# Optimization experiments

Hardware: AMD Instinct MI355X
Metric: run time of the kernel (lower is better)

Reference implementation:

```python
import jax, jax.numpy as jnp
import numpy as np

B, H_HIST, S_DIM, HID, G, K, A = 1024, 16384, 32, 64, 10, 4, 8


def setup_inputs() -> dict:
    key = jax.random.key(0)
    ks = jax.random.split(key, 12)
    inp = {
        'state_batch': jax.random.normal(ks[0], (B, S_DIM), jnp.float32),
        'state_history_batch': jax.random.normal(ks[1], (H_HIST, S_DIM), jnp.float32),
        'joint_action_history_batch': jax.random.normal(ks[2], (H_HIST, G, A), jnp.float32),
        # per-abstract-agent encoder MLP: Linear(S->H) + ReLU, Linear(H->H) + ReLU, Linear(H->H) + ReLU
        'W0': jax.random.normal(ks[3], (K, S_DIM, HID), jnp.float32) / np.sqrt(S_DIM),
        'b0': jax.random.normal(ks[4], (K, HID), jnp.float32) * 0.01,
        'W1': jax.random.normal(ks[5], (K, HID, HID), jnp.float32) / np.sqrt(HID),
        'b1': jax.random.normal(ks[6], (K, HID), jnp.float32) * 0.01,
        'W2': jax.random.normal(ks[7], (K, HID, HID), jnp.float32) / np.sqrt(HID),
        'b2': jax.random.normal(ks[8], (K, HID), jnp.float32) * 0.01,
        'assignment_matrix': jnp.ones((G, K), jnp.float32),
    }
    return inp


def _encode(x, W0, b0, W1, b1, W2, b2):
    # x: [N, S_DIM] shared across K encoders -> [K, N, HID]
    h = jax.nn.relu(jnp.einsum('ni,kio->kno', x, W0) + b0[:, None, :])
    h = jax.nn.relu(jnp.einsum('kni,kio->kno', h, W1) + b1[:, None, :])
    h = jax.nn.relu(jnp.einsum('kni,kio->kno', h, W2) + b2[:, None, :])
    return h


def reference(state_batch, state_history_batch, joint_action_history_batch,
              W0, b0, W1, b1, W2, b2, assignment_matrix):
    enc_s = _encode(state_batch, W0, b0, W1, b1, W2, b2)            # [K, B, HID]
    enc_h = _encode(state_history_batch, W0, b0, W1, b1, W2, b2)    # [K, H, HID]
    # per (abstract agent k, batch item b): softmax over history of <enc_h, enc_s>
    attn = jax.nn.softmax(jnp.einsum('khd,kbd->kbh', enc_h, enc_s), axis=-1)  # [K, B, H]
    # weighted action aggregation: [H,G,A] contracted over H
    abs_pred = jnp.einsum('kbh,hga->kbga', attn, joint_action_history_batch)  # [K, B, G, A]
    soft_assign = jax.nn.softmax(assignment_matrix, axis=-1)                  # [G, K]
    out = jnp.einsum('gk,kbga->bga', soft_assign, abs_pred)                   # [B, G, A]
    return out
```

## Files before the change

kernel.cpp:

```cpp
#include <hip/hip_runtime.h>
#include <stdint.h>

#define B_SZ 1024
#define H_SZ 16384
#define SD   32
#define HID  64
#define G_SZ 10
#define K_SZ 4
#define A_SZ 8
#define VA   80

typedef float f32x4  __attribute__((ext_vector_type(4)));
typedef short bf16x8 __attribute__((ext_vector_type(8)));

__device__ inline short f2bf(float a) {
    unsigned u = __float_as_uint(a);
    return (short)((u + 0x7FFFu + ((u >> 16) & 1u)) >> 16);
}
__device__ inline float bf2f(short s) {
    return __uint_as_float(((unsigned)(unsigned short)s) << 16);
}
__device__ inline void split_bf(float v, short& hi, short& lo) {
    hi = f2bf(v);
    lo = f2bf(v - bf2f(hi));
}
__device__ inline int cvt_pk_bf16(float a, float b) {
    int r;
    asm("v_cvt_pk_bf16_f32 %0, %1, %2" : "=v"(r) : "v"(a), "v"(b));
    return r;
}

__global__ __launch_bounds__(256) void k_prep(
    const float* __restrict__ W0, const float* __restrict__ W1,
    const float* __restrict__ W2,
    short* __restrict__ w0h, short* __restrict__ w0l,
    short* __restrict__ w1h, short* __restrict__ w1l,
    short* __restrict__ w2h, short* __restrict__ w2l)
{
    int idx = blockIdx.x * 256 + threadIdx.x;
    short hh, ll;
    if (idx < 8192) {
        int k = idx >> 11, j = (idx >> 5) & 63, i = idx & 31;
        split_bf(W0[k * 2048 + i * 64 + j], hh, ll);
        w0h[idx] = hh; w0l[idx] = ll;
    } else if (idx < 24576) {
        int d = idx - 8192;
        int k = d >> 12, j = (d >> 6) & 63, i = d & 63;
        split_bf(W1[k * 4096 + i * 64 + j], hh, ll);
        w1h[d] = hh; w1l[d] = ll;
    } else if (idx < 40960) {
        int d = idx - 24576;
        int k = d >> 12, j = (d >> 6) & 63, i = d & 63;
        split_bf(W2[k * 4096 + i * 64 + j], hh, ll);
        w2h[d] = hh; w2l[d] = ll;
    }
}

__global__ __launch_bounds__(256, 2) void k_encode(
    const float* __restrict__ state, const float* __restrict__ hist,
    const float* __restrict__ act,
    const short* __restrict__ w0th, const short* __restrict__ w0tl,
    const short* __restrict__ w1th, const short* __restrict__ w1tl,
    const short* __restrict__ w2th, const short* __restrict__ w2tl,
    const float* __restrict__ b0, const float* __restrict__ b1,
    const float* __restrict__ b2,
    short* __restrict__ enc_s_h, short* __restrict__ enc_s_l,
    short* __restrict__ kf_h, short* __restrict__ kf_l,
    short* __restrict__ vf_h, short* __restrict__ vf_l)
{
    __shared__ __align__(16) short smem[28672];
    const int bid = blockIdx.x;
    const int t = threadIdx.x;

    if (bid >= 1088) {
        short* tile_h = smem;
        short* tile_l = smem + 10752;
        const int h0 = (bid - 1088) * 128;
        for (int i = 0; i < 40; ++i) {
            int idx = t + i * 256;
            float v = act[(size_t)h0 * VA + idx];
            int h = idx / VA, c = idx - h * VA;
            short hh, ll; split_bf(v, hh, ll);
            tile_h[h * 84 + c] = hh;
            tile_l[h * 84 + c] = ll;
        }
        __syncthreads();
        for (int i = 0; i < 5; ++i) {
            int j = t + i * 256;
            int va = j >> 4, hc = j & 15;
            union { short s[8]; uint4 v; } uh, ul;
            #pragma unroll
            for (int uu = 0; uu < 8; ++uu) {
                uh.s[uu] = tile_h[(hc * 8 + uu) * 84 + va];
                ul.s[uu] = tile_l[(hc * 8 + uu) * 84 + va];
            }
            int vtile = (h0 >> 5) + (hc >> 2);
            int lanep = ((hc & 3) << 4) | (va & 15);
            size_t a = (size_t)vtile * 2560 + (va >> 4) * 512 + lanep * 8;
            *(uint4*)(vf_h + a) = uh.v;
            *(uint4*)(vf_l + a) = ul.v;
        }
        return;
    }

    const int k = bid / 272;
    const int tl = bid % 272;
    const bool is_state = (tl < 16);
    const float qscale = is_state ? 1.44269504f : 1.0f;
    const float* X;
    short *dst_h = nullptr, *dst_l = nullptr;
    if (is_state) {
        X = state + (size_t)tl * 64 * SD;
        dst_h = enc_s_h + ((size_t)k * B_SZ + tl * 64) * HID;
        dst_l = enc_s_l + ((size_t)k * B_SZ + tl * 64) * HID;
    } else {
        X = hist + (size_t)(tl - 16) * 64 * SD;
    }

    short* xt_h  = smem;
    short* xt_l  = smem + 2560;
    short* wt0_h = smem + 5120;
    short* wt0_l = smem + 7680;
    short* hb2_h = smem;
    short* hb2_l = smem + 4608;
    short* wt1_h = smem + 10240;
    short* wt1_l = smem + 14848;
    short* ot_h  = smem + 10240;
    short* ot_l  = smem + 14848;
    short* hb1_h = smem + 19456;
    short* hb1_l = smem + 24064;
    short* wt2_h = smem + 19456;
    short* wt2_l = smem + 24064;

    {
        int r = t >> 2, c0 = (t & 3) * 8;
        const float* src = X + r * SD + c0;
        #pragma unroll
        for (int u = 0; u < 8; ++u) {
            short hh, ll; split_bf(src[u], hh, ll);
            xt_h[r * 40 + c0 + u] = hh;
            xt_l[r * 40 + c0 + u] = ll;
        }
    }
    {
        int jj = t >> 2, i0 = (t & 3) * 8;
        *(uint4*)(wt0_h + jj * 40 + i0) = *(const uint4*)(w0th + k * 2048 + jj * 32 + i0);
        *(uint4*)(wt0_l + jj * 40 + i0) = *(const uint4*)(w0tl + k * 2048 + jj * 32 + i0);
    }
    {
        int jj = t >> 2, i0 = (t & 3) * 16;
        *(uint4*)(wt1_h + jj * 72 + i0)     = *(const uint4*)(w1th + k * 4096 + jj * 64 + i0);
        *(uint4*)(wt1_h + jj * 72 + i0 + 8) = *(const uint4*)(w1th + k * 4096 + jj * 64 + i0 + 8);
        *(uint4*)(wt1_l + jj * 72 + i0)     = *(const uint4*)(w1tl + k * 4096 + jj * 64 + i0);
        *(uint4*)(wt1_l + jj * 72 + i0 + 8) = *(const uint4*)(w1tl + k * 4096 + jj * 64 + i0 + 8);
    }
    __syncthreads();

    const int w = t >> 6, l15 = t & 15, quad = (t >> 4) & 3;
    const f32x4 fz = {0.f, 0.f, 0.f, 0.f};

    {
        bf16x8 xa_h = *(const bf16x8*)(xt_h + (w * 16 + l15) * 40 + quad * 8);
        bf16x8 xa_l = *(const bf16x8*)(xt_l + (w * 16 + l15) * 40 + quad * 8);
        const float* b0k = b0 + k * HID;
        #pragma unroll
        for (int tt = 0; tt < 4; ++tt) {
            bf16x8 wf_h = *(const bf16x8*)(wt0_h + (l15 + 16 * tt) * 40 + quad * 8);
            bf16x8 wf_l = *(const bf16x8*)(wt0_l + (l15 + 16 * tt) * 40 + quad * 8);
            f32x4 c = __builtin_amdgcn_mfma_f32_16x16x32_bf16(xa_h, wf_h, fz, 0, 0, 0);
            c = __builtin_amdgcn_mfma_f32_16x16x32_bf16(xa_l, wf_h, c, 0, 0, 0);
            c = __builtin_amdgcn_mfma_f32_16x16x32_bf16(xa_h, wf_l, c, 0, 0, 0);
            float bias = b0k[l15 + 16 * tt];
            #pragma unroll
            for (int r = 0; r < 4; ++r) {
                float f = fmaxf(c[r] + bias, 0.f);
                short hh, ll; split_bf(f, hh, ll);
                hb1_h[(w * 16 + quad * 4 + r) * 72 + l15 + 16 * tt] = hh;
                hb1_l[(w * 16 + quad * 4 + r) * 72 + l15 + 16 * tt] = ll;
            }
        }
    }
    __syncthreads();
    {
        bf16x8 ha0_h = *(const bf16x8*)(hb1_h + (w * 16 + l15) * 72 + quad * 8);
        bf16x8 ha0_l = *(const bf16x8*)(hb1_l + (w * 16 + l15) * 72 + quad * 8);
        bf16x8 ha1_h = *(const bf16x8*)(hb1_h + (w * 16 + l15) * 72 + 32 + quad * 8);
        bf16x8 ha1_l = *(const bf16x8*)(hb1_l + (w * 16 + l15) * 72 + 32 + quad * 8);
        const float* b1k = b1 + k * HID;
        #pragma unroll
        for (int tt = 0; tt < 4; ++tt) {
            bf16x8 wfa_h = *(const bf16x8*)(wt1_h + (l15 + 16 * tt) * 72 + quad * 8);
            bf16x8 wfa_l = *(const bf16x8*)(wt1_l + (l15 + 16 * tt) * 72 + quad * 8);
            bf16x8 wfb_h = *(const bf16x8*)(wt1_h + (l15 + 16 * tt) * 72 + 32 + quad * 8);
            bf16x8 wfb_l = *(const bf16x8*)(wt1_l + (l15 + 16 * tt) * 72 + 32 + quad * 8);
            f32x4 c = __builtin_amdgcn_mfma_f32_16x16x32_bf16(ha0_h, wfa_h, fz, 0, 0, 0);
            c = __builtin_amdgcn_mfma_f32_16x16x32_bf16(ha1_h, wfb_h, c, 0, 0, 0);
            c = __builtin_amdgcn_mfma_f32_16x16x32_bf16(ha0_l, wfa_h, c, 0, 0, 0);
            c = __builtin_amdgcn_mfma_f32_16x16x32_bf16(ha1_l, wfb_h, c, 0, 0, 0);
            c = __builtin_amdgcn_mfma_f32_16x16x32_bf16(ha0_h, wfa_l, c, 0, 0, 0);
            c = __builtin_amdgcn_mfma_f32_16x16x32_bf16(ha1_h, wfb_l, c, 0, 0, 0);
            float bias = b1k[l15 + 16 * tt];
            #pragma unroll
            for (int r = 0; r < 4; ++r) {
                float f = fmaxf(c[r] + bias, 0.f);
                short hh, ll; split_bf(f, hh, ll);
                hb2_h[(w * 16 + quad * 4 + r) * 72 + l15 + 16 * tt] = hh;
                hb2_l[(w * 16 + quad * 4 + r) * 72 + l15 + 16 * tt] = ll;
            }
        }
    }
    __syncthreads();
    {
        int jj = t >> 2, i0 = (t & 3) * 16;
        *(uint4*)(wt2_h + jj * 72 + i0)     = *(const uint4*)(w2th + k * 4096 + jj * 64 + i0);
        *(uint4*)(wt2_h + jj * 72 + i0 + 8) = *(const uint4*)(w2th + k * 4096 + jj * 64 + i0 + 8);
        *(uint4*)(wt2_l + jj * 72 + i0)     = *(const uint4*)(w2tl + k * 4096 + jj * 64 + i0);
        *(uint4*)(wt2_l + jj * 72 + i0 + 8) = *(const uint4*)(w2tl + k * 4096 + jj * 64 + i0 + 8);
    }
    __syncthreads();
    {
        bf16x8 ha0_h = *(const bf16x8*)(hb2_h + (w * 16 + l15) * 72 + quad * 8);
        bf16x8 ha0_l = *(const bf16x8*)(hb2_l + (w * 16 + l15) * 72 + quad * 8);
        bf16x8 ha1_h = *(const bf16x8*)(hb2_h + (w * 16 + l15) * 72 + 32 + quad * 8);
        bf16x8 ha1_l = *(const bf16x8*)(hb2_l + (w * 16 + l15) * 72 + 32 + quad * 8);
        const float* b2k = b2 + k * HID;
        #pragma unroll
        for (int tt = 0; tt < 4; ++tt) {
            bf16x8 wfa_h = *(const bf16x8*)(wt2_h + (l15 + 16 * tt) * 72 + quad * 8);
            bf16x8 wfa_l = *(const bf16x8*)(wt2_l + (l15 + 16 * tt) * 72 + quad * 8);
            bf16x8 wfb_h = *(const bf16x8*)(wt2_h + (l15 + 16 * tt) * 72 + 32 + quad * 8);
            bf16x8 wfb_l = *(const bf16x8*)(wt2_l + (l15 + 16 * tt) * 72 + 32 + quad * 8);
            f32x4 c = __builtin_amdgcn_mfma_f32_16x16x32_bf16(ha0_h, wfa_h, fz, 0, 0, 0);
            c = __builtin_amdgcn_mfma_f32_16x16x32_bf16(ha1_h, wfb_h, c, 0, 0, 0);
            c = __builtin_amdgcn_mfma_f32_16x16x32_bf16(ha0_l, wfa_h, c, 0, 0, 0);
            c = __builtin_amdgcn_mfma_f32_16x16x32_bf16(ha1_l, wfb_h, c, 0, 0, 0);
            c = __builtin_amdgcn_mfma_f32_16x16x32_bf16(ha0_h, wfa_l, c, 0, 0, 0);
            c = __builtin_amdgcn_mfma_f32_16x16x32_bf16(ha1_h, wfb_l, c, 0, 0, 0);
            float bias = b2k[l15 + 16 * tt];
            #pragma unroll
            for (int r = 0; r < 4; ++r) {
                float f = fmaxf(c[r] + bias, 0.f) * qscale;
                short hh, ll; split_bf(f, hh, ll);
                int row = w * 16 + quad * 4 + r;
                int col = l15 + 16 * tt;
                ot_h[row * 72 + col] = hh;
                ot_l[row * 72 + col] = ll;
            }
        }
    }
    __syncthreads();
    if (is_state) {
        #pragma unroll
        for (int u = 0; u < 2; ++u) {
            int id = t * 2 + u;
            int row = id >> 3, c0 = (id & 7) * 8;
            *(uint4*)(dst_h + row * HID + c0) = *(const uint4*)(ot_h + row * 72 + c0);
            *(uint4*)(dst_l + row * HID + c0) = *(const uint4*)(ot_l + row * 72 + c0);
        }
    } else {
        const int ktbase = k * 512 + (tl - 16) * 2;
        #pragma unroll
        for (int u = 0; u < 2; ++u) {
            int id = t * 2 + u;
            int kt2 = id >> 8;
            int f2 = (id >> 6) & 3;
            int lanep = id & 63;
            int hl = kt2 * 32 + ((f2 >> 1) & 1) * 16 + (lanep & 15);
            int c0 = (f2 & 1) * 32 + ((lanep >> 4) & 3) * 8;
            size_t a = (size_t)(ktbase + kt2) * 2048 + f2 * 512 + (size_t)lanep * 8;
            *(uint4*)(kf_h + a) = *(const uint4*)(ot_h + hl * 72 + c0);
            *(uint4*)(kf_l + a) = *(const uint4*)(ot_l + hl * 72 + c0);
        }
    }
}

template<int NCt>
__global__ __launch_bounds__(256, 2) void k_flash(
    const short* __restrict__ enc_s_h, const short* __restrict__ enc_s_l,
    const short* __restrict__ kf_h, const short* __restrict__ kf_l,
    const short* __restrict__ vf_h, const short* __restrict__ vf_l,
    float* __restrict__ Pm, float* __restrict__ Pl, float* __restrict__ Pacc)
{
    constexpr int CHt = H_SZ / NCt;
    constexpr int NT = CHt / 32;
    static_assert(NT % 2 == 0, "NT must be even for 2x unroll");

    const int bid = blockIdx.x;
    const int r8 = bid & 7, j = bid >> 3;
    const int mtile = j & 7, grp = j >> 3;
    const int idx = grp * 8 + r8;
    const int k = idx / NCt, chunk = idx % NCt;
    const int t = threadIdx.x, w = t >> 6, lane = t & 63;
    const int l15 = t & 15, quad = (t >> 4) & 3;
    const int q0 = mtile * 128 + w * 32;
    const f32x4 fz = {0.f, 0.f, 0.f, 0.f};

    bf16x8 qh[2][2], ql[2][2];
    #pragma unroll
    for (int sub = 0; sub < 2; ++sub)
        #pragma unroll
        for (int kb = 0; kb < 2; ++kb) {
            size_t off = ((size_t)k * B_SZ + q0 + sub * 16 + l15) * HID + kb * 32 + quad * 8;
            qh[sub][kb] = *(const bf16x8*)(enc_s_h + off);
            ql[sub][kb] = *(const bf16x8*)(enc_s_l + off);
        }

    f32x4 acc[2][5];
    #pragma unroll
    for (int s = 0; s < 2; ++s)
        #pragma unroll
        for (int tt = 0; tt < 5; ++tt) acc[s][tt] = fz;
    float mrun[2] = {-__builtin_inff(), -__builtin_inff()};
    float lrun[2] = {0.f, 0.f};

    const int tile0 = chunk * NT;
    const short* kbh = kf_h + ((size_t)(k * 512 + tile0)) * 2048 + lane * 8;
    const short* kbl = kf_l + ((size_t)(k * 512 + tile0)) * 2048 + lane * 8;
    const short* vbh = vf_h + (size_t)tile0 * 2560 + lane * 8;
    const short* vbl = vf_l + (size_t)tile0 * 2560 + lane * 8;

    bf16x8 kA[8], kB[8];
    #pragma unroll
    for (int f = 0; f < 4; ++f) {
        kA[f]     = *(const bf16x8*)(kbh + f * 512);
        kA[4 + f] = *(const bf16x8*)(kbl + f * 512);
    }

    auto body = [&](bf16x8 (&kc)[8], bf16x8 (&kn)[8], int it) {
        bf16x8 vh[5], vl[5];
        const short* vph = vbh + (size_t)it * 2560;
        const short* vpl = vbl + (size_t)it * 2560;
        #pragma unroll
        for (int tt = 0; tt < 3; ++tt) {
            vh[tt] = *(const bf16x8*)(vph + tt * 512);
            vl[tt] = *(const bf16x8*)(vpl + tt * 512);
        }
        if (it + 1 < NT) {
            const short* nph = kbh + (size_t)(it + 1) * 2048;
            const short* npl = kbl + (size_t)(it + 1) * 2048;
            #pragma unroll
            for (int f = 0; f < 4; ++f) {
                kn[f]     = *(const bf16x8*)(nph + f * 512);
                kn[4 + f] = *(const bf16x8*)(npl + f * 512);
            }
        }

        f32x4 S[2][2];
        __builtin_amdgcn_s_setprio(1);
        #pragma unroll
        for (int sub = 0; sub < 2; ++sub) {
            f32x4 c = __builtin_amdgcn_mfma_f32_16x16x32_bf16(kc[0], qh[sub][0], fz, 0, 0, 0);
            c = __builtin_amdgcn_mfma_f32_16x16x32_bf16(kc[1], qh[sub][1], c, 0, 0, 0);
            c = __builtin_amdgcn_mfma_f32_16x16x32_bf16(kc[4], qh[sub][0], c, 0, 0, 0);
            c = __builtin_amdgcn_mfma_f32_16x16x32_bf16(kc[5], qh[sub][1], c, 0, 0, 0);
            c = __builtin_amdgcn_mfma_f32_16x16x32_bf16(kc[0], ql[sub][0], c, 0, 0, 0);
            c = __builtin_amdgcn_mfma_f32_16x16x32_bf16(kc[1], ql[sub][1], c, 0, 0, 0);
            S[sub][0] = c;
            f32x4 d = __builtin_amdgcn_mfma_f32_16x16x32_bf16(kc[2], qh[sub][0], fz, 0, 0, 0);
            d = __builtin_amdgcn_mfma_f32_16x16x32_bf16(kc[3], qh[sub][1], d, 0, 0, 0);
            d = __builtin_amdgcn_mfma_f32_16x16x32_bf16(kc[6], qh[sub][0], d, 0, 0, 0);
            d = __builtin_amdgcn_mfma_f32_16x16x32_bf16(kc[7], qh[sub][1], d, 0, 0, 0);
            d = __builtin_amdgcn_mfma_f32_16x16x32_bf16(kc[2], ql[sub][0], d, 0, 0, 0);
            d = __builtin_amdgcn_mfma_f32_16x16x32_bf16(kc[3], ql[sub][1], d, 0, 0, 0);
            S[sub][1] = d;
        }
        __builtin_amdgcn_s_setprio(0);

        #pragma unroll
        for (int tt = 3; tt < 5; ++tt) {
            vh[tt] = *(const bf16x8*)(vph + tt * 512);
            vl[tt] = *(const bf16x8*)(vpl + tt * 512);
        }

        bf16x8 pfv[2];
        #pragma unroll
        for (int sub = 0; sub < 2; ++sub) {
            f32x4 slo = S[sub][0], shi = S[sub][1];
            float a3 = fmaxf(fmaxf(slo[0], slo[1]), slo[2]);
            float b3 = fmaxf(fmaxf(slo[3], shi[0]), shi[1]);
            float c3 = fmaxf(fmaxf(shi[2], shi[3]), a3);
            float tm = fmaxf(b3, c3);
            tm = fmaxf(tm, __shfl_xor(tm, 16));
            tm = fmaxf(tm, __shfl_xor(tm, 32));
            if (__any(tm > mrun[sub])) {
                float mnew = fmaxf(mrun[sub], tm);
                float alpha = exp2f(mrun[sub] - mnew);
                lrun[sub] *= alpha;
                #pragma unroll
                for (int tt = 0; tt < 5; ++tt) acc[sub][tt] = acc[sub][tt] * alpha;
                mrun[sub] = mnew;
            }
            float m = mrun[sub];
            float p0 = exp2f(slo[0] - m), p1 = exp2f(slo[1] - m);
            float p2 = exp2f(slo[2] - m), p3 = exp2f(slo[3] - m);
            float p4 = exp2f(shi[0] - m), p5 = exp2f(shi[1] - m);
            float p6 = exp2f(shi[2] - m), p7 = exp2f(shi[3] - m);
            float ps = (p0 + p1) + (p2 + p3) + (p4 + p5) + (p6 + p7);
            ps += __shfl_xor(ps, 16);
            ps += __shfl_xor(ps, 32);
            lrun[sub] += ps;

            int plo01 = cvt_pk_bf16(p0, p1), plo23 = cvt_pk_bf16(p2, p3);
            int phi01 = cvt_pk_bf16(p4, p5), phi23 = cvt_pk_bf16(p6, p7);
            union { int i[4]; bf16x8 v; } pf;
            #pragma unroll
            for (int jj = 0; jj < 4; ++jj) {
                int src = (((2 * quad + (jj >> 1)) & 3) << 4) + l15;
                int glo = __shfl((jj & 1) ? plo23 : plo01, src);
                int ghi = __shfl((jj & 1) ? phi23 : phi01, src);
                pf.i[jj] = (quad >= 2) ? ghi : glo;
            }
            pfv[sub] = pf.v;
        }

        __builtin_amdgcn_s_setprio(1);
        #pragma unroll
        for (int tt = 0; tt < 5; ++tt) {
            acc[0][tt] = __builtin_amdgcn_mfma_f32_16x16x32_bf16(vh[tt], pfv[0], acc[0][tt], 0, 0, 0);
            acc[0][tt] = __builtin_amdgcn_mfma_f32_16x16x32_bf16(vl[tt], pfv[0], acc[0][tt], 0, 0, 0);
            acc[1][tt] = __builtin_amdgcn_mfma_f32_16x16x32_bf16(vh[tt], pfv[1], acc[1][tt], 0, 0, 0);
            acc[1][tt] = __builtin_amdgcn_mfma_f32_16x16x32_bf16(vl[tt], pfv[1], acc[1][tt], 0, 0, 0);
        }
        __builtin_amdgcn_s_setprio(0);
    };

    for (int ii = 0; ii < NT; ii += 2) {
        body(kA, kB, ii);
        body(kB, kA, ii + 1);
    }

    const int qg = k * B_SZ + q0;
    #pragma unroll
    for (int sub = 0; sub < 2; ++sub) {
        int q = qg + sub * 16 + l15;
        if (quad == 0) {
            Pm[chunk * 4096 + q] = mrun[sub];
            Pl[chunk * 4096 + q] = lrun[sub];
        }
        #pragma unroll
        for (int tt = 0; tt < 5; ++tt)
            #pragma unroll
            for (int r = 0; r < 4; ++r) {
                int va = tt * 16 + quad * 4 + r;
                Pacc[((size_t)chunk * VA + va) * 4096 + q] = acc[sub][tt][r];
            }
    }
}

template<int NCt>
__global__ __launch_bounds__(256) void k_reduce1(
    const float* __restrict__ Pm, const float* __restrict__ Pl,
    const float* __restrict__ Pacc, float* __restrict__ O)
{
    const int bid = blockIdx.x;
    const int qb = bid / 10, vc = bid - qb * 10;
    const int t = threadIdx.x;
    const int q = qb * 64 + (t & 63);
    const int va0 = vc * 8 + (t >> 6) * 2;

    float mc[NCt];
    float M = -__builtin_inff();
    #pragma unroll
    for (int c = 0; c < NCt; ++c) { mc[c] = Pm[c * 4096 + q]; M = fmaxf(M, mc[c]); }
    float L = 0.f;
    float o0 = 0.f, o1 = 0.f;
    #pragma unroll
    for (int c = 0; c < NCt; ++c) {
        float wv = exp2f(mc[c] - M);
        L += wv * Pl[c * 4096 + q];
        o0 += wv * Pacc[((size_t)c * VA + va0) * 4096 + q];
        o1 += wv * Pacc[((size_t)c * VA + va0 + 1) * 4096 + q];
    }
    float inv = 1.f / L;
    O[(size_t)q * VA + va0]     = o0 * inv;
    O[(size_t)q * VA + va0 + 1] = o1 * inv;
}

__global__ __launch_bounds__(256) void k_reduce2(
    const float* __restrict__ O, const float* __restrict__ assign,
    float* __restrict__ out)
{
    const int idx = blockIdx.x * 256 + threadIdx.x;
    const int b = idx / VA, va = idx - b * VA, g = va >> 3;
    const float L2E = 1.44269504f;
    float a0 = assign[g * K_SZ + 0], a1 = assign[g * K_SZ + 1];
    float a2 = assign[g * K_SZ + 2], a3 = assign[g * K_SZ + 3];
    float mx = fmaxf(fmaxf(a0, a1), fmaxf(a2, a3));
    float e0 = exp2f((a0 - mx) * L2E), e1 = exp2f((a1 - mx) * L2E);
    float e2 = exp2f((a2 - mx) * L2E), e3 = exp2f((a3 - mx) * L2E);
    float inv = 1.f / (e0 + e1 + e2 + e3);
    float o = e0 * O[((size_t)(0 * B_SZ + b)) * VA + va]
            + e1 * O[((size_t)(1 * B_SZ + b)) * VA + va]
            + e2 * O[((size_t)(2 * B_SZ + b)) * VA + va]
            + e3 * O[((size_t)(3 * B_SZ + b)) * VA + va];
    out[idx] = o * inv;
}

extern "C" void kernel_launch(void* const* d_in, const int* in_sizes, int n_in,
                              void* d_out, int out_size, void* d_ws, size_t ws_size,
                              hipStream_t stream)
{
    const float* state  = (const float*)d_in[0];
    const float* hist   = (const float*)d_in[1];
    const float* act    = (const float*)d_in[2];
    const float* W0     = (const float*)d_in[3];
    const float* b0     = (const float*)d_in[4];
    const float* W1     = (const float*)d_in[5];
    const float* b1     = (const float*)d_in[6];
    const float* W2     = (const float*)d_in[7];
    const float* b2     = (const float*)d_in[8];
    const float* assign = (const float*)d_in[9];
    float* out = (float*)d_out;

    char* ws = (char*)d_ws;
    short* enc_s_h = (short*)(ws);
    short* enc_s_l = (short*)(ws + 524288);
    short* kf_h    = (short*)(ws + 1048576);
    short* kf_l    = (short*)(ws + 9437184);
    short* vf_h    = (short*)(ws + 17825792);
    short* vf_l    = (short*)(ws + 20447232);
    const size_t base = 23068672;

    const size_t need32 = base + 32ull * (32768 + 1310720) + 1310720 + 163840;
    const int nc = (ws_size >= need32) ? 32 : 16;

    float* Pm   = (float*)(ws + base);
    float* Pl   = (float*)(ws + base + (size_t)nc * 16384);
    float* Pacc = (float*)(ws + base + (size_t)nc * 32768);
    float* O    = (float*)(ws + base + (size_t)nc * 32768 + (size_t)nc * 1310720);
    char*  wt   = (char*)O + 1310720;
    short* w0th = (short*)(wt);
    short* w0tl = (short*)(wt + 16384);
    short* w1th = (short*)(wt + 32768);
    short* w1tl = (short*)(wt + 65536);
    short* w2th = (short*)(wt + 98304);
    short* w2tl = (short*)(wt + 131072);

    k_prep<<<160, 256, 0, stream>>>(W0, W1, W2, w0th, w0tl, w1th, w1tl, w2th, w2tl);
    k_encode<<<1216, 256, 0, stream>>>(state, hist, act,
                                       w0th, w0tl, w1th, w1tl, w2th, w2tl,
                                       b0, b1, b2,
                                       enc_s_h, enc_s_l, kf_h, kf_l, vf_h, vf_l);
    if (nc == 32) {
        k_flash<32><<<1024, 256, 0, stream>>>(enc_s_h, enc_s_l, kf_h, kf_l,
                                              vf_h, vf_l, Pm, Pl, Pacc);
        k_reduce1<32><<<640, 256, 0, stream>>>(Pm, Pl, Pacc, O);
    } else {
        k_flash<16><<<512, 256, 0, stream>>>(enc_s_h, enc_s_l, kf_h, kf_l,
                                             vf_h, vf_l, Pm, Pl, Pacc);
        k_reduce1<16><<<640, 256, 0, stream>>>(Pm, Pl, Pacc, O);
    }
    k_reduce2<<<320, 256, 0, stream>>>(O, assign, out);
}
```

Before: 167.4 us.

## Pre-swizzle encoder weights into MFMA fragment order and load directly from global

```diff
diff --git a/kernel.cpp b/kernel.cpp
--- a/kernel.cpp
+++ b/kernel.cpp
@@ -17,17 +17,20 @@
     unsigned u = __float_as_uint(a);
     return (short)((u + 0x7FFFu + ((u >> 16) & 1u)) >> 16);
 }
-__device__ inline float bf2f(short s) {
-    return __uint_as_float(((unsigned)(unsigned short)s) << 16);
-}
 __device__ inline void split_bf(float v, short& hi, short& lo) {
     hi = f2bf(v);
-    lo = f2bf(v - bf2f(hi));
+    lo = f2bf(v - __uint_as_float(((unsigned)(unsigned short)hi) << 16));
 }
 __device__ inline int cvt_pk_bf16(float a, float b) {
     int r;
     asm("v_cvt_pk_bf16_f32 %0, %1, %2" : "=v"(r) : "v"(a), "v"(b));
     return r;
+}
+__device__ inline void split2(float f0, float f1, int& hi, int& lo) {
+    hi = cvt_pk_bf16(f0, f1);
+    float r0 = f0 - __uint_as_float((unsigned)hi << 16);
+    float r1 = f1 - __uint_as_float((unsigned)hi & 0xFFFF0000u);
+    lo = cvt_pk_bf16(r0, r1);
 }
 
 __global__ __launch_bounds__(256) void k_prep(
@@ -40,65 +43,81 @@
     int idx = blockIdx.x * 256 + threadIdx.x;
     short hh, ll;
     if (idx < 8192) {
-        int k = idx >> 11, j = (idx >> 5) & 63, i = idx & 31;
-        split_bf(W0[k * 2048 + i * 64 + j], hh, ll);
-        w0h[idx] = hh; w0l[idx] = ll;
+        int k = idx >> 11, r = idx & 2047;
+        int i = r >> 6, jj = r & 63;
+        int tt = jj >> 4, l15 = jj & 15;
+        int quad = (i >> 3) & 3, e = i & 7;
+        split_bf(W0[k * 2048 + i * 64 + jj], hh, ll);
+        int dst = k * 2048 + tt * 512 + (quad * 16 + l15) * 8 + e;
+        w0h[dst] = hh; w0l[dst] = ll;
     } else if (idx < 24576) {
         int d = idx - 8192;
-        int k = d >> 12, j = (d >> 6) & 63, i = d & 63;
-        split_bf(W1[k * 4096 + i * 64 + j], hh, ll);
-        w1h[d] = hh; w1l[d] = ll;
+        int k = d >> 12, r = d & 4095;
+        int i = r >> 6, jj = r & 63;
+        int kb = i >> 5, quad = (i >> 3) & 3, e = i & 7;
+        int tt = jj >> 4, l15 = jj & 15;
+        split_bf(W1[k * 4096 + i * 64 + jj], hh, ll);
+        int dst = k * 4096 + tt * 1024 + kb * 512 + (quad * 16 + l15) * 8 + e;
+        w1h[dst] = hh; w1l[dst] = ll;
     } else if (idx < 40960) {
         int d = idx - 24576;
-        int k = d >> 12, j = (d >> 6) & 63, i = d & 63;
-        split_bf(W2[k * 4096 + i * 64 + j], hh, ll);
-        w2h[d] = hh; w2l[d] = ll;
-    }
-}
-
-__global__ __launch_bounds__(256, 2) void k_encode(
+        int k = d >> 12, r = d & 4095;
+        int i = r >> 6, jj = r & 63;
+        int kb = i >> 5, quad = (i >> 3) & 3, e = i & 7;
+        int tt = jj >> 4, l15 = jj & 15;
+        split_bf(W2[k * 4096 + i * 64 + jj], hh, ll);
+        int dst = k * 4096 + tt * 1024 + kb * 512 + (quad * 16 + l15) * 8 + e;
+        w2h[dst] = hh; w2l[dst] = ll;
+    }
+}
+
+__global__ __launch_bounds__(256, 3) void k_encode(
     const float* __restrict__ state, const float* __restrict__ hist,
     const float* __restrict__ act,
-    const short* __restrict__ w0th, const short* __restrict__ w0tl,
-    const short* __restrict__ w1th, const short* __restrict__ w1tl,
-    const short* __restrict__ w2th, const short* __restrict__ w2tl,
+    const short* __restrict__ w0fh, const short* __restrict__ w0fl,
+    const short* __restrict__ w1fh, const short* __restrict__ w1fl,
+    const short* __restrict__ w2fh, const short* __restrict__ w2fl,
     const float* __restrict__ b0, const float* __restrict__ b1,
     const float* __restrict__ b2,
     short* __restrict__ enc_s_h, short* __restrict__ enc_s_l,
     short* __restrict__ kf_h, short* __restrict__ kf_l,
     short* __restrict__ vf_h, short* __restrict__ vf_l)
 {
-    __shared__ __align__(16) short smem[28672];
+    __shared__ __align__(16) short smem[18432];
     const int bid = blockIdx.x;
     const int t = threadIdx.x;
 
     if (bid >= 1088) {
         short* tile_h = smem;
-        short* tile_l = smem + 10752;
-        const int h0 = (bid - 1088) * 128;
-        for (int i = 0; i < 40; ++i) {
-            int idx = t + i * 256;
-            float v = act[(size_t)h0 * VA + idx];
-            int h = idx / VA, c = idx - h * VA;
-            short hh, ll; split_bf(v, hh, ll);
-            tile_h[h * 84 + c] = hh;
-            tile_l[h * 84 + c] = ll;
+        short* tile_l = smem + 5376;
+        const int h0 = (bid - 1088) * 64;
+        #pragma unroll
+        for (int i = 0; i < 10; ++i) {
+            int idx2 = 2 * (t + i * 256);
+            float2 v = *(const float2*)(act + (size_t)h0 * VA + idx2);
+            int h = idx2 / 80, c = idx2 - h * 80;
+            int hi, lo; split2(v.x, v.y, hi, lo);
+            *(int*)(tile_h + h * 84 + c) = hi;
+            *(int*)(tile_l + h * 84 + c) = lo;
         }
         __syncthreads();
-        for (int i = 0; i < 5; ++i) {
-            int j = t + i * 256;
-            int va = j >> 4, hc = j & 15;
-            union { short s[8]; uint4 v; } uh, ul;
-            #pragma unroll
-            for (int uu = 0; uu < 8; ++uu) {
-                uh.s[uu] = tile_h[(hc * 8 + uu) * 84 + va];
-                ul.s[uu] = tile_l[(hc * 8 + uu) * 84 + va];
+        #pragma unroll
+        for (int i = 0; i < 3; ++i) {
+            int jj = t + i * 256;
+            if (jj < 640) {
+                int va = jj >> 3, hb = jj & 7;
+                union { short s[8]; uint4 v; } uh, ul;
+                #pragma unroll
+                for (int uu = 0; uu < 8; ++uu) {
+                    uh.s[uu] = tile_h[(hb * 8 + uu) * 84 + va];
+                    ul.s[uu] = tile_l[(hb * 8 + uu) * 84 + va];
+                }
+                int vtile = (h0 >> 5) + (hb >> 2);
+                int lanep = ((hb & 3) << 4) | (va & 15);
+                size_t a = (size_t)vtile * 2560 + (va >> 4) * 512 + lanep * 8;
+                *(uint4*)(vf_h + a) = uh.v;
+                *(uint4*)(vf_l + a) = ul.v;
             }
-            int vtile = (h0 >> 5) + (hc >> 2);
-            int lanep = ((hc & 3) << 4) | (va & 15);
-            size_t a = (size_t)vtile * 2560 + (va >> 4) * 512 + lanep * 8;
-            *(uint4*)(vf_h + a) = uh.v;
-            *(uint4*)(vf_l + a) = ul.v;
         }
         return;
     }
@@ -107,77 +126,64 @@
     const int tl = bid % 272;
     const bool is_state = (tl < 16);
     const float qscale = is_state ? 1.44269504f : 1.0f;
-    const float* X;
-    short *dst_h = nullptr, *dst_l = nullptr;
-    if (is_state) {
-        X = state + (size_t)tl * 64 * SD;
-        dst_h = enc_s_h + ((size_t)k * B_SZ + tl * 64) * HID;
-        dst_l = enc_s_l + ((size_t)k * B_SZ + tl * 64) * HID;
-    } else {
-        X = hist + (size_t)(tl - 16) * 64 * SD;
-    }
+    const float* X = is_state ? state + (size_t)tl * 64 * SD
+                              : hist + (size_t)(tl - 16) * 64 * SD;
+    short* dst_h = enc_s_h + ((size_t)k * B_SZ + tl * 64) * HID;
+    short* dst_l = enc_s_l + ((size_t)k * B_SZ + tl * 64) * HID;
 
     short* xt_h  = smem;
     short* xt_l  = smem + 2560;
-    short* wt0_h = smem + 5120;
-    short* wt0_l = smem + 7680;
     short* hb2_h = smem;
     short* hb2_l = smem + 4608;
-    short* wt1_h = smem + 10240;
-    short* wt1_l = smem + 14848;
-    short* ot_h  = smem + 10240;
-    short* ot_l  = smem + 14848;
-    short* hb1_h = smem + 19456;
-    short* hb1_l = smem + 24064;
-    short* wt2_h = smem + 19456;
-    short* wt2_l = smem + 24064;
+    short* hb1_h = smem + 9216;
+    short* hb1_l = smem + 13824;
+    short* ot_h  = smem + 9216;
+    short* ot_l  = smem + 13824;
 
     {
         int r = t >> 2, c0 = (t & 3) * 8;
         const float* src = X + r * SD + c0;
         #pragma unroll
-        for (int u = 0; u < 8; ++u) {
-            short hh, ll; split_bf(src[u], hh, ll);
-            xt_h[r * 40 + c0 + u] = hh;
-            xt_l[r * 40 + c0 + u] = ll;
-        }
-    }
-    {
-        int jj = t >> 2, i0 = (t & 3) * 8;
-        *(uint4*)(wt0_h + jj * 40 + i0) = *(const uint4*)(w0th + k * 2048 + jj * 32 + i0);
-        *(uint4*)(wt0_l + jj * 40 + i0) = *(const uint4*)(w0tl + k * 2048 + jj * 32 + i0);
-    }
-    {
-        int jj = t >> 2, i0 = (t & 3) * 16;
-        *(uint4*)(wt1_h + jj * 72 + i0)     = *(const uint4*)(w1th + k * 4096 + jj * 64 + i0);
-        *(uint4*)(wt1_h + jj * 72 + i0 + 8) = *(const uint4*)(w1th + k * 4096 + jj * 64 + i0 + 8);
-        *(uint4*)(wt1_l + jj * 72 + i0)     = *(const uint4*)(w1tl + k * 4096 + jj * 64 + i0);
-        *(uint4*)(wt1_l + jj * 72 + i0 + 8) = *(const uint4*)(w1tl + k * 4096 + jj * 64 + i0 + 8);
+        for (int u = 0; u < 4; ++u) {
+            float2 v = *(const float2*)(src + 2 * u);
+            int hi, lo; split2(v.x, v.y, hi, lo);
+            *(int*)(xt_h + r * 40 + c0 + 2 * u) = hi;
+            *(int*)(xt_l + r * 40 + c0 + 2 * u) = lo;
+        }
     }
     __syncthreads();
 
-    const int w = t >> 6, l15 = t & 15, quad = (t >> 4) & 3;
+    const int w = t >> 6, l15 = t & 15, quad = (t >> 4) & 3, lane = t & 63;
     const f32x4 fz = {0.f, 0.f, 0.f, 0.f};
+    const int row0 = w * 16 + quad * 4;
 
     {
         bf16x8 xa_h = *(const bf16x8*)(xt_h + (w * 16 + l15) * 40 + quad * 8);
         bf16x8 xa_l = *(const bf16x8*)(xt_l + (w * 16 + l15) * 40 + quad * 8);
         const float* b0k = b0 + k * HID;
+        const short* wbh = w0fh + k * 2048 + lane * 8;
+        const short* wbl = w0fl + k * 2048 + lane * 8;
         #pragma unroll
         for (int tt = 0; tt < 4; ++tt) {
-            bf16x8 wf_h = *(const bf16x8*)(wt0_h + (l15 + 16 * tt) * 40 + quad * 8);
-            bf16x8 wf_l = *(const bf16x8*)(wt0_l + (l15 + 16 * tt) * 40 + quad * 8);
+            bf16x8 wf_h = *(const bf16x8*)(wbh + tt * 512);
+            bf16x8 wf_l = *(const bf16x8*)(wbl + tt * 512);
             f32x4 c = __builtin_amdgcn_mfma_f32_16x16x32_bf16(xa_h, wf_h, fz, 0, 0, 0);
             c = __builtin_amdgcn_mfma_f32_16x16x32_bf16(xa_l, wf_h, c, 0, 0, 0);
             c = __builtin_amdgcn_mfma_f32_16x16x32_bf16(xa_h, wf_l, c, 0, 0, 0);
             float bias = b0k[l15 + 16 * tt];
-            #pragma unroll
-            for (int r = 0; r < 4; ++r) {
-                float f = fmaxf(c[r] + bias, 0.f);
-                short hh, ll; split_bf(f, hh, ll);
-                hb1_h[(w * 16 + quad * 4 + r) * 72 + l15 + 16 * tt] = hh;
-                hb1_l[(w * 16 + quad * 4 + r) * 72 + l15 + 16 * tt] = ll;
-            }
+            float f0 = fmaxf(c[0] + bias, 0.f), f1 = fmaxf(c[1] + bias, 0.f);
+            float f2 = fmaxf(c[2] + bias, 0.f), f3 = fmaxf(c[3] + bias, 0.f);
+            int h01, l01, h23, l23;
+            split2(f0, f1, h01, l01); split2(f2, f3, h23, l23);
+            int cc = l15 + 16 * tt;
+            hb1_h[(row0    ) * 72 + cc] = (short)h01;
+            hb1_h[(row0 + 1) * 72 + cc] = (short)(h01 >> 16);
+            hb1_h[(row0 + 2) * 72 + cc] = (short)h23;
+            hb1_h[(row0 + 3) * 72 + cc] = (short)(h23 >> 16);
+            hb1_l[(row0    ) * 72 + cc] = (short)l01;
+            hb1_l[(row0 + 1) * 72 + cc] = (short)(l01 >> 16);
+            hb1_l[(row0 + 2) * 72 + cc] = (short)l23;
+            hb1_l[(row0 + 3) * 72 + cc] = (short)(l23 >> 16);
         }
     }
     __syncthreads();
@@ -187,12 +193,14 @@
         bf16x8 ha1_h = *(const bf16x8*)(hb1_h + (w * 16 + l15) * 72 + 32 + quad * 8);
         bf16x8 ha1_l = *(const bf16x8*)(hb1_l + (w * 16 + l15) * 72 + 32 + quad * 8);
         const float* b1k = b1 + k * HID;
+        const short* wbh = w1fh + k * 4096 + lane * 8;
+        const short* wbl = w1fl + k * 4096 + lane * 8;
         #pragma unroll
         for (int tt = 0; tt < 4; ++tt) {
-            bf16x8 wfa_h = *(const bf16x8*)(wt1_h + (l15 + 16 * tt) * 72 + quad * 8);
-            bf16x8 wfa_l = *(const bf16x8*)(wt1_l + (l15 + 16 * tt) * 72 + quad * 8);
-            bf16x8 wfb_h = *(const bf16x8*)(wt1_h + (l15 + 16 * tt) * 72 + 32 + quad * 8);
-            bf16x8 wfb_l = *(const bf16x8*)(wt1_l + (l15 + 16 * tt) * 72 + 32 + quad * 8);
+            bf16x8 wfa_h = *(const bf16x8*)(wbh + tt * 1024);
+            bf16x8 wfb_h = *(const bf16x8*)(wbh + tt * 1024 + 512);
+            bf16x8 wfa_l = *(const bf16x8*)(wbl + tt * 1024);
+            bf16x8 wfb_l = *(const bf16x8*)(wbl + tt * 1024 + 512);
             f32x4 c = __builtin_amdgcn_mfma_f32_16x16x32_bf16(ha0_h, wfa_h, fz, 0, 0, 0);
             c = __builtin_amdgcn_mfma_f32_16x16x32_bf16(ha1_h, wfb_h, c, 0, 0, 0);
             c = __builtin_amdgcn_mfma_f32_16x16x32_bf16(ha0_l, wfa_h, c, 0, 0, 0);
@@ -200,22 +208,20 @@
             c = __builtin_amdgcn_mfma_f32_16x16x32_bf16(ha0_h, wfa_l, c, 0, 0, 0);
             c = __builtin_amdgcn_mfma_f32_16x16x32_bf16(ha1_h, wfb_l, c, 0, 0, 0);
             float bias = b1k[l15 + 16 * tt];
-            #pragma unroll
-            for (int r = 0; r < 4; ++r) {
-                float f = fmaxf(c[r] + bias, 0.f);
-                short hh, ll; split_bf(f, hh, ll);
-                hb2_h[(w * 16 + quad * 4 + r) * 72 + l15 + 16 * tt] = hh;
-                hb2_l[(w * 16 + quad * 4 + r) * 72 + l15 + 16 * tt] = ll;
-            }
-        }
-    }
-    __syncthreads();
-    {
-        int jj = t >> 2, i0 = (t & 3) * 16;
-        *(uint4*)(wt2_h + jj * 72 + i0)     = *(const uint4*)(w2th + k * 4096 + jj * 64 + i0);
-        *(uint4*)(wt2_h + jj * 72 + i0 + 8) = *(const uint4*)(w2th + k * 4096 + jj * 64 + i0 + 8);
-        *(uint4*)(wt2_l + jj * 72 + i0)     = *(const uint4*)(w2tl + k * 4096 + jj * 64 + i0);
-        *(uint4*)(wt2_l + jj * 72 + i0 + 8) = *(const uint4*)(w2tl + k * 4096 + jj * 64 + i0 + 8);
+            float f0 = fmaxf(c[0] + bias, 0.f), f1 = fmaxf(c[1] + bias, 0.f);
+            float f2 = fmaxf(c[2] + bias, 0.f), f3 = fmaxf(c[3] + bias, 0.f);
+            int h01, l01, h23, l23;
+            split2(f0, f1, h01, l01); split2(f2, f3, h23, l23);
+            int cc = l15 + 16 * tt;
+            hb2_h[(row0    ) * 72 + cc] = (short)h01;
+            hb2_h[(row0 + 1) * 72 + cc] = (short)(h01 >> 16);
+            hb2_h[(row0 + 2) * 72 + cc] = (short)h23;
+            hb2_h[(row0 + 3) * 72 + cc] = (short)(h23 >> 16);
+            hb2_l[(row0    ) * 72 + cc] = (short)l01;
+            hb2_l[(row0 + 1) * 72 + cc] = (short)(l01 >> 16);
+            hb2_l[(row0 + 2) * 72 + cc] = (short)l23;
+            hb2_l[(row0 + 3) * 72 + cc] = (short)(l23 >> 16);
+        }
     }
     __syncthreads();
     {
@@ -224,12 +230,14 @@
         bf16x8 ha1_h = *(const bf16x8*)(hb2_h + (w * 16 + l15) * 72 + 32 + quad * 8);
         bf16x8 ha1_l = *(const bf16x8*)(hb2_l + (w * 16 + l15) * 72 + 32 + quad * 8);
         const float* b2k = b2 + k * HID;
+        const short* wbh = w2fh + k * 4096 + lane * 8;
+        const short* wbl = w2fl + k * 4096 + lane * 8;
         #pragma unroll
         for (int tt = 0; tt < 4; ++tt) {
-            bf16x8 wfa_h = *(const bf16x8*)(wt2_h + (l15 + 16 * tt) * 72 + quad * 8);
-            bf16x8 wfa_l = *(const bf16x8*)(wt2_l + (l15 + 16 * tt) * 72 + quad * 8);
-            bf16x8 wfb_h = *(const bf16x8*)(wt2_h + (l15 + 16 * tt) * 72 + 32 + quad * 8);
-            bf16x8 wfb_l = *(const bf16x8*)(wt2_l + (l15 + 16 * tt) * 72 + 32 + quad * 8);
+            bf16x8 wfa_h = *(const bf16x8*)(wbh + tt * 1024);
+            bf16x8 wfb_h = *(const bf16x8*)(wbh + tt * 1024 + 512);
+            bf16x8 wfa_l = *(const bf16x8*)(wbl + tt * 1024);
+            bf16x8 wfb_l = *(const bf16x8*)(wbl + tt * 1024 + 512);
             f32x4 c = __builtin_amdgcn_mfma_f32_16x16x32_bf16(ha0_h, wfa_h, fz, 0, 0, 0);
             c = __builtin_amdgcn_mfma_f32_16x16x32_bf16(ha1_h, wfb_h, c, 0, 0, 0);
             c = __builtin_amdgcn_mfma_f32_16x16x32_bf16(ha0_l, wfa_h, c, 0, 0, 0);
@@ -237,15 +245,21 @@
             c = __builtin_amdgcn_mfma_f32_16x16x32_bf16(ha0_h, wfa_l, c, 0, 0, 0);
             c = __builtin_amdgcn_mfma_f32_16x16x32_bf16(ha1_h, wfb_l, c, 0, 0, 0);
             float bias = b2k[l15 + 16 * tt];
-            #pragma unroll
-            for (int r = 0; r < 4; ++r) {
-                float f = fmaxf(c[r] + bias, 0.f) * qscale;
-                short hh, ll; split_bf(f, hh, ll);
-                int row = w * 16 + quad * 4 + r;
-                int col = l15 + 16 * tt;
-                ot_h[row * 72 + col] = hh;
-                ot_l[row * 72 + col] = ll;
-            }
+            float f0 = fmaxf(c[0] + bias, 0.f) * qscale;
+            float f1 = fmaxf(c[1] + bias, 0.f) * qscale;
+            float f2 = fmaxf(c[2] + bias, 0.f) * qscale;
+            float f3 = fmaxf(c[3] + bias, 0.f) * qscale;
+            int h01, l01, h23, l23;
+            split2(f0, f1, h01, l01); split2(f2, f3, h23, l23);
+            int cc = l15 + 16 * tt;
+            ot_h[(row0    ) * 72 + cc] = (short)h01;
+            ot_h[(row0 + 1) * 72 + cc] = (short)(h01 >> 16);
+            ot_h[(row0 + 2) * 72 + cc] = (short)h23;
+            ot_h[(row0 + 3) * 72 + cc] = (short)(h23 >> 16);
+            ot_l[(row0    ) * 72 + cc] = (short)l01;
+            ot_l[(row0 + 1) * 72 + cc] = (short)(l01 >> 16);
+            ot_l[(row0 + 2) * 72 + cc] = (short)l23;
+            ot_l[(row0 + 3) * 72 + cc] = (short)(l23 >> 16);
         }
     }
     __syncthreads();
@@ -529,16 +543,16 @@
     float* Pacc = (float*)(ws + base + (size_t)nc * 32768);
     float* O    = (float*)(ws + base + (size_t)nc * 32768 + (size_t)nc * 1310720);
     char*  wt   = (char*)O + 1310720;
-    short* w0th = (short*)(wt);
-    short* w0tl = (short*)(wt + 16384);
-    short* w1th = (short*)(wt + 32768);
-    short* w1tl = (short*)(wt + 65536);
-    short* w2th = (short*)(wt + 98304);
-    short* w2tl = (short*)(wt + 131072);
-
-    k_prep<<<160, 256, 0, stream>>>(W0, W1, W2, w0th, w0tl, w1th, w1tl, w2th, w2tl);
-    k_encode<<<1216, 256, 0, stream>>>(state, hist, act,
-                                       w0th, w0tl, w1th, w1tl, w2th, w2tl,
+    short* w0fh = (short*)(wt);
+    short* w0fl = (short*)(wt + 16384);
+    short* w1fh = (short*)(wt + 32768);
+    short* w1fl = (short*)(wt + 65536);
+    short* w2fh = (short*)(wt + 98304);
+    short* w2fl = (short*)(wt + 131072);
+
+    k_prep<<<160, 256, 0, stream>>>(W0, W1, W2, w0fh, w0fl, w1fh, w1fl, w2fh, w2fl);
+    k_encode<<<1344, 256, 0, stream>>>(state, hist, act,
+                                       w0fh, w0fl, w1fh, w1fl, w2fh, w2fl,
                                        b0, b1, b2,
                                        enc_s_h, enc_s_l, kf_h, kf_l, vf_h, vf_l);
     if (nc == 32) {
```

After: 164.2 us. About the same (-1.9%).
